# Kernel optimization log

Measured on AMD Instinct MI355X. Metric: run time of the kernel, lower is better.

## Reference

```python
import jax, jax.numpy as jnp
import numpy as np

N_NODES = 50000
N_EDGES = 800000
IN_CH, HID_CH, OUT_CH = 128, 128, 64


def setup_inputs() -> dict:
    key = jax.random.key(0)
    ks = jax.random.split(key, 8)
    x = jax.random.normal(ks[0], (N_NODES, IN_CH), dtype=jnp.float32)
    src = jax.random.randint(ks[1], (N_EDGES,), 0, N_NODES, dtype=jnp.int32)
    dst = jax.random.randint(ks[2], (N_EDGES,), 0, N_NODES, dtype=jnp.int32)
    s1 = 1.0 / np.sqrt(IN_CH)
    s2 = 1.0 / np.sqrt(HID_CH)
    W_self1 = jax.random.normal(ks[3], (IN_CH, HID_CH), dtype=jnp.float32) * s1
    W_neigh1 = jax.random.normal(ks[4], (IN_CH, HID_CH), dtype=jnp.float32) * s1
    b1 = jnp.zeros((HID_CH,), dtype=jnp.float32)
    W_self2 = jax.random.normal(ks[5], (HID_CH, OUT_CH), dtype=jnp.float32) * s2
    W_neigh2 = jax.random.normal(ks[6], (HID_CH, OUT_CH), dtype=jnp.float32) * s2
    b2 = jnp.zeros((OUT_CH,), dtype=jnp.float32)
    return {"x": x, "src": src, "dst": dst,
            "W_self1": W_self1, "W_neigh1": W_neigh1, "b1": b1,
            "W_self2": W_self2, "W_neigh2": W_neigh2, "b2": b2}


def _mean_agg(h, src, dst, inv_deg):
    # gather source features, scatter-sum onto destinations, divide by in-degree
    summed = jax.ops.segment_sum(h[src], dst, num_segments=N_NODES)  # [N, d]
    return summed * inv_deg[:, None]


def _sage_layer(h, src, dst, inv_deg, W_self, W_neigh, b):
    h_neigh = _mean_agg(h, src, dst, inv_deg)
    return h @ W_self + h_neigh @ W_neigh + b


def reference(x, src, dst, W_self1, W_neigh1, b1, W_self2, W_neigh2, b2):
    deg = jax.ops.segment_sum(jnp.ones_like(dst, dtype=x.dtype), dst,
                              num_segments=N_NODES)
    inv_deg = 1.0 / jnp.maximum(deg, 1.0)  # isolated nodes -> 0 neighbor feature
    h = _sage_layer(x, src, dst, inv_deg, W_self1, W_neigh1, b1)
    h = jax.nn.relu(h)
    out = _sage_layer(h, src, dst, inv_deg, W_self2, W_neigh2, b2)
    return out
```

## Files before the change

kernel.cpp:

```cpp
#include <hip/hip_runtime.h>

#define N_CH 128
#define CAP 7680

typedef short bf16x8 __attribute__((ext_vector_type(8)));
typedef float f32x4 __attribute__((ext_vector_type(4)));

__device__ __forceinline__ unsigned short f2bf(float f) {
    unsigned int u = __float_as_uint(f);
    unsigned int r = (u + 0x7fffu + ((u >> 16) & 1u)) >> 16;
    return (unsigned short)r;
}
__device__ __forceinline__ unsigned int pkbf(float a, float b) {
    return (unsigned int)f2bf(a) | ((unsigned int)f2bf(b) << 16);
}
__device__ __forceinline__ float bflo(unsigned int v) { return __uint_as_float(v << 16); }
__device__ __forceinline__ float bfhi(unsigned int v) { return __uint_as_float(v & 0xffff0000u); }

__global__ __launch_bounds__(256) void k_inithist(const float* __restrict__ x,
                                                  const float* __restrict__ Ws1,
                                                  const float* __restrict__ Wn1,
                                                  const float* __restrict__ Ws2,
                                                  const float* __restrict__ Wn2,
                                                  unsigned short* __restrict__ Bt1,
                                                  unsigned short* __restrict__ Bt2,
                                                  uint4* __restrict__ xb4, int nxq, int nxb,
                                                  const int* __restrict__ dst,
                                                  int* __restrict__ H, int e, int nbh,
                                                  int nbkt) {
    __shared__ int hist[256];
    int b = blockIdx.x, t = threadIdx.x;
    if (b < 192) {
        int idx = b * 256 + t;
        if (idx < 128 * 256) {
            int n = idx >> 8, k = idx & 255;
            float v = (k < 128) ? Ws1[k * 128 + n] : Wn1[(k - 128) * 128 + n];
            Bt1[idx] = f2bf(v);
        } else {
            int j = idx - 128 * 256;
            int n = j >> 7, k = j & 127;
            float v = (n < 64) ? Ws2[k * 64 + n] : Wn2[k * 64 + (n - 64)];
            Bt2[j] = f2bf(v);
        }
    } else if (b < 192 + nxb) {
        int q = (b - 192) * 256 + t;
        if (q < nxq) {
            const float4* xf = (const float4*)x;
            float4 f0 = xf[2 * q], f1 = xf[2 * q + 1];
            uint4 o;
            o.x = pkbf(f0.x, f0.y); o.y = pkbf(f0.z, f0.w);
            o.z = pkbf(f1.x, f1.y); o.w = pkbf(f1.z, f1.w);
            xb4[q] = o;
        }
    } else {
        int hb = b - 192 - nxb;
        hist[t] = 0;
        __syncthreads();
        int i = hb * 1024 + t * 4;
        if (i + 3 < e) {
            int4 d4 = *(const int4*)&dst[i];
            atomicAdd(&hist[d4.x >> 8], 1);
            atomicAdd(&hist[d4.y >> 8], 1);
            atomicAdd(&hist[d4.z >> 8], 1);
            atomicAdd(&hist[d4.w >> 8], 1);
        } else {
            for (int j = i; j < e && j < i + 4; ++j) atomicAdd(&hist[dst[j] >> 8], 1);
        }
        __syncthreads();
        if (t < nbkt) H[t * nbh + hb] = hist[t];
    }
}

__global__ __launch_bounds__(256) void k_reduce(const int* __restrict__ H,
                                                int* __restrict__ bsum, int tot) {
    __shared__ int sm[256];
    int i = blockIdx.x * 256 + threadIdx.x;
    sm[threadIdx.x] = (i < tot) ? H[i] : 0;
    __syncthreads();
    for (int s = 128; s > 0; s >>= 1) {
        if (threadIdx.x < s) sm[threadIdx.x] += sm[threadIdx.x + s];
        __syncthreads();
    }
    if (threadIdx.x == 0) bsum[blockIdx.x] = sm[0];
}

__global__ __launch_bounds__(256) void k_scan(const int* __restrict__ H,
                                              const int* __restrict__ bsum,
                                              int* __restrict__ Hs, int tot) {
    __shared__ int sm[256];
    __shared__ int sbase;
    int t = threadIdx.x, b = blockIdx.x;
    int acc = 0;
    for (int j = t; j < b; j += 256) acc += bsum[j];
    sm[t] = acc;
    __syncthreads();
    for (int s = 128; s > 0; s >>= 1) {
        if (t < s) sm[t] += sm[t + s];
        __syncthreads();
    }
    if (t == 0) sbase = sm[0];
    __syncthreads();
    int base = sbase;
    __syncthreads();
    int i = b * 256 + t;
    int v = (i < tot) ? H[i] : 0;
    sm[t] = v;
    __syncthreads();
    for (int off = 1; off < 256; off <<= 1) {
        int add = (t >= off) ? sm[t - off] : 0;
        __syncthreads();
        sm[t] += add;
        __syncthreads();
    }
    if (i < tot) Hs[i] = base + sm[t] - v;
}

__global__ __launch_bounds__(256) void k_scatter1(const int* __restrict__ src,
                                                  const int* __restrict__ dst,
                                                  const int* __restrict__ Hs,
                                                  int* __restrict__ buf,
                                                  int e, int nbh, int nbkt) {
    __shared__ int cur[256];
    int t = threadIdx.x, b = blockIdx.x;
    if (t < nbkt) cur[t] = Hs[t * nbh + b];
    __syncthreads();
    int i = b * 1024 + t * 4;
    if (i + 3 < e) {
        int4 d4 = *(const int4*)&dst[i];
        int4 s4 = *(const int4*)&src[i];
        int r0 = atomicAdd(&cur[d4.x >> 8], 1);
        buf[r0] = ((d4.x & 255) << 16) | s4.x;
        int r1 = atomicAdd(&cur[d4.y >> 8], 1);
        buf[r1] = ((d4.y & 255) << 16) | s4.y;
        int r2 = atomicAdd(&cur[d4.z >> 8], 1);
        buf[r2] = ((d4.z & 255) << 16) | s4.z;
        int r3 = atomicAdd(&cur[d4.w >> 8], 1);
        buf[r3] = ((d4.w & 255) << 16) | s4.w;
    } else {
        for (int j = i; j < e && j < i + 4; ++j) {
            int d = dst[j];
            int r = atomicAdd(&cur[d >> 8], 1);
            buf[r] = ((d & 255) << 16) | src[j];
        }
    }
}

__global__ __launch_bounds__(256) void k_bucket(const int* __restrict__ buf,
                                                const int* __restrict__ Hs,
                                                int* __restrict__ csr_src,
                                                int* __restrict__ deg,
                                                int* __restrict__ row_start,
                                                int e, int nbh, int nbkt, int n) {
    __shared__ int hist[256];
    __shared__ int excl[256];
    __shared__ int cur[256];
    __shared__ int cache[CAP];
    int t = threadIdx.x, b = blockIdx.x;
    int base = Hs[b * nbh];
    int end = (b == nbkt - 1) ? e : Hs[(b + 1) * nbh];
    int cnt = end - base;
    hist[t] = 0;
    __syncthreads();
    for (int i = t; i < cnt; i += 256) {
        int v = buf[base + i];
        if (i < CAP) cache[i] = v;
        atomicAdd(&hist[(v >> 16) & 255], 1);
    }
    __syncthreads();
    int v = hist[t];
    excl[t] = v;
    __syncthreads();
    for (int off = 1; off < 256; off <<= 1) {
        int add = (t >= off) ? excl[t - off] : 0;
        __syncthreads();
        excl[t] += add;
        __syncthreads();
    }
    int ex = excl[t] - v;
    cur[t] = ex;
    int node = b * 256 + t;
    if (node < n) {
        deg[node] = v;
        row_start[node] = base + ex;
    }
    __syncthreads();
    for (int i = t; i < cnt; i += 256) {
        int ed = (i < CAP) ? cache[i] : buf[base + i];
        int r = atomicAdd(&cur[(ed >> 16) & 255], 1);
        csr_src[base + r] = ed & 0xFFFF;
    }
}

__global__ __launch_bounds__(256) void k_aggx(const uint4* __restrict__ xb4,
                                              uint4* __restrict__ xagg4,
                                              const int* __restrict__ row_start,
                                              const int* __restrict__ deg,
                                              const int* __restrict__ csr, int n) {
    int gw = (blockIdx.x * 256 + threadIdx.x) >> 6;
    int lane = threadIdx.x & 63;
    if (gw >= n) return;
    int start = row_start[gw];
    int cnt = deg[gw];
    const int q = lane >> 4;
    const int cl = lane & 15;
    float a0 = 0.f, a1 = 0.f, a2 = 0.f, a3 = 0.f, a4 = 0.f, a5 = 0.f, a6 = 0.f, a7 = 0.f;
    int i = 0;
    for (; i + 16 <= cnt; i += 16) {
        int e0 = csr[start + i + q];
        int e1 = csr[start + i + 4 + q];
        int e2 = csr[start + i + 8 + q];
        int e3 = csr[start + i + 12 + q];
        uint4 v0 = xb4[e0 * 16 + cl];
        uint4 v1 = xb4[e1 * 16 + cl];
        uint4 v2 = xb4[e2 * 16 + cl];
        uint4 v3 = xb4[e3 * 16 + cl];
        a0 += bflo(v0.x) + bflo(v1.x) + bflo(v2.x) + bflo(v3.x);
        a1 += bfhi(v0.x) + bfhi(v1.x) + bfhi(v2.x) + bfhi(v3.x);
        a2 += bflo(v0.y) + bflo(v1.y) + bflo(v2.y) + bflo(v3.y);
        a3 += bfhi(v0.y) + bfhi(v1.y) + bfhi(v2.y) + bfhi(v3.y);
        a4 += bflo(v0.z) + bflo(v1.z) + bflo(v2.z) + bflo(v3.z);
        a5 += bfhi(v0.z) + bfhi(v1.z) + bfhi(v2.z) + bfhi(v3.z);
        a6 += bflo(v0.w) + bflo(v1.w) + bflo(v2.w) + bflo(v3.w);
        a7 += bfhi(v0.w) + bfhi(v1.w) + bfhi(v2.w) + bfhi(v3.w);
    }
    if (i + 8 <= cnt) {
        int e0 = csr[start + i + q];
        int e1 = csr[start + i + 4 + q];
        uint4 v0 = xb4[e0 * 16 + cl];
        uint4 v1 = xb4[e1 * 16 + cl];
        a0 += bflo(v0.x) + bflo(v1.x); a1 += bfhi(v0.x) + bfhi(v1.x);
        a2 += bflo(v0.y) + bflo(v1.y); a3 += bfhi(v0.y) + bfhi(v1.y);
        a4 += bflo(v0.z) + bflo(v1.z); a5 += bfhi(v0.z) + bfhi(v1.z);
        a6 += bflo(v0.w) + bflo(v1.w); a7 += bfhi(v0.w) + bfhi(v1.w);
        i += 8;
    }
    for (; i < cnt; i += 4) {
        int nbi = i + q;
        if (nbi < cnt) {
            uint4 va = xb4[csr[start + nbi] * 16 + cl];
            a0 += bflo(va.x); a1 += bfhi(va.x);
            a2 += bflo(va.y); a3 += bfhi(va.y);
            a4 += bflo(va.z); a5 += bfhi(va.z);
            a6 += bflo(va.w); a7 += bfhi(va.w);
        }
    }
    a0 += __shfl_xor(a0, 16); a0 += __shfl_xor(a0, 32);
    a1 += __shfl_xor(a1, 16); a1 += __shfl_xor(a1, 32);
    a2 += __shfl_xor(a2, 16); a2 += __shfl_xor(a2, 32);
    a3 += __shfl_xor(a3, 16); a3 += __shfl_xor(a3, 32);
    a4 += __shfl_xor(a4, 16); a4 += __shfl_xor(a4, 32);
    a5 += __shfl_xor(a5, 16); a5 += __shfl_xor(a5, 32);
    a6 += __shfl_xor(a6, 16); a6 += __shfl_xor(a6, 32);
    a7 += __shfl_xor(a7, 16); a7 += __shfl_xor(a7, 32);

    float inv = 1.0f / fmaxf((float)cnt, 1.0f);
    if (q == 0) {
        uint4 o;
        o.x = pkbf(inv * a0, inv * a1);
        o.y = pkbf(inv * a2, inv * a3);
        o.z = pkbf(inv * a4, inv * a5);
        o.w = pkbf(inv * a6, inv * a7);
        xagg4[gw * 16 + cl] = o;
    }
}

__global__ __launch_bounds__(256) void k_gemm12(const uint4* __restrict__ xb4,
                                                const uint4* __restrict__ xagg4,
                                                const unsigned short* __restrict__ Bt1,
                                                const float* __restrict__ b1,
                                                const unsigned short* __restrict__ Bt2,
                                                const float* __restrict__ b2,
                                                float* __restrict__ out,
                                                unsigned short* __restrict__ p2, int M) {
    __shared__ unsigned short As[64][256];
    unsigned short* lds = &As[0][0];
    const int m0 = blockIdx.x * 64;
    const int tid = threadIdx.x;
    const int w = tid >> 6;
    const int l = tid & 63;
    const int fr = l & 15;
    const int kq = l >> 4;

    for (int p = tid; p < 2048; p += 256) {
        int row = p >> 5, c = p & 31;
        int gr = m0 + row;
        uint4 v = make_uint4(0, 0, 0, 0);
        if (gr < M) v = (c < 16) ? xb4[gr * 16 + c] : xagg4[gr * 16 + (c - 16)];
        *(uint4*)&As[row][(c ^ (row & 7)) * 8] = v;
    }
    __syncthreads();

    f32x4 acc[2][4] = {};
#pragma unroll
    for (int kt = 0; kt < 8; ++kt) {
        bf16x8 bfr[2];
#pragma unroll
        for (int ct = 0; ct < 2; ++ct) {
            int nn = w * 32 + ct * 16 + fr;
            bfr[ct] = *(const bf16x8*)&Bt1[nn * 256 + kt * 32 + kq * 8];
        }
        bf16x8 af[4];
#pragma unroll
        for (int rt = 0; rt < 4; ++rt) {
            int row = rt * 16 + fr;
            int c = (kt * 4 + kq) ^ (row & 7);
            af[rt] = *(bf16x8*)&As[row][c * 8];
        }
#pragma unroll
        for (int ct = 0; ct < 2; ++ct)
#pragma unroll
            for (int rt = 0; rt < 4; ++rt)
                acc[ct][rt] = __builtin_amdgcn_mfma_f32_16x16x32_bf16(af[rt], bfr[ct],
                                                                      acc[ct][rt], 0, 0, 0);
    }
    __syncthreads();

#pragma unroll
    for (int ct = 0; ct < 2; ++ct) {
        int col = w * 32 + ct * 16 + fr;
        float bv = b1[col];
        int c8 = col >> 3, c7 = col & 7;
#pragma unroll
        for (int rt = 0; rt < 4; ++rt) {
#pragma unroll
            for (int j = 0; j < 4; ++j) {
                int row = rt * 16 + (l >> 4) * 4 + j;
                unsigned short hv = f2bf(fmaxf(acc[ct][rt][j] + bv, 0.f));
                lds[row * 128 + (c8 ^ (row & 7)) * 8 + c7] = hv;
            }
        }
    }
    __syncthreads();

    f32x4 acc2[2][4] = {};
#pragma unroll
    for (int kt = 0; kt < 4; ++kt) {
        bf16x8 bfr[2];
#pragma unroll
        for (int ct = 0; ct < 2; ++ct) {
            int nn = w * 32 + ct * 16 + fr;
            bfr[ct] = *(const bf16x8*)&Bt2[nn * 128 + kt * 32 + kq * 8];
        }
        bf16x8 af[4];
#pragma unroll
        for (int rt = 0; rt < 4; ++rt) {
            int row = rt * 16 + fr;
            int c = (kt * 4 + kq) ^ (row & 7);
            af[rt] = *(bf16x8*)&lds[row * 128 + c * 8];
        }
#pragma unroll
        for (int ct = 0; ct < 2; ++ct)
#pragma unroll
            for (int rt = 0; rt < 4; ++rt)
                acc2[ct][rt] = __builtin_amdgcn_mfma_f32_16x16x32_bf16(af[rt], bfr[ct],
                                                                       acc2[ct][rt], 0, 0, 0);
    }

#pragma unroll
    for (int ct = 0; ct < 2; ++ct) {
        int col = w * 32 + ct * 16 + fr;
        bool isS = col < 64;
        float bv = isS ? b2[col] : 0.f;
#pragma unroll
        for (int rt = 0; rt < 4; ++rt) {
#pragma unroll
            for (int j = 0; j < 4; ++j) {
                int row = m0 + rt * 16 + (l >> 4) * 4 + j;
                if (row < M) {
                    float v = acc2[ct][rt][j];
                    if (isS) out[row * 64 + col] = v + bv;
                    else p2[row * 64 + (col - 64)] = f2bf(v);
                }
            }
        }
    }
}

__global__ __launch_bounds__(256) void k_agg2_add(const unsigned int* __restrict__ p,
                                                  float* __restrict__ out,
                                                  const int* __restrict__ row_start,
                                                  const int* __restrict__ deg,
                                                  const int* __restrict__ csr, int n) {
    int gw = (blockIdx.x * 256 + threadIdx.x) >> 6;
    int lane = threadIdx.x & 63;
    if (gw >= n) return;
    int start = row_start[gw];
    int cnt = deg[gw];
    const int g = lane >> 3;
    const int cl = lane & 7;
    float a0 = 0.f, a1 = 0.f, a2 = 0.f, a3 = 0.f, a4 = 0.f, a5 = 0.f, a6 = 0.f, a7 = 0.f;
    int i = 0;
    for (; i + 16 <= cnt; i += 16) {
        int e0 = csr[start + i + g];
        int e1 = csr[start + i + 8 + g];
        uint4 v0 = *(const uint4*)&p[e0 * 32 + cl * 4];
        uint4 v1 = *(const uint4*)&p[e1 * 32 + cl * 4];
        a0 += bflo(v0.x) + bflo(v1.x); a1 += bfhi(v0.x) + bfhi(v1.x);
        a2 += bflo(v0.y) + bflo(v1.y); a3 += bfhi(v0.y) + bfhi(v1.y);
        a4 += bflo(v0.z) + bflo(v1.z); a5 += bfhi(v0.z) + bfhi(v1.z);
        a6 += bflo(v0.w) + bflo(v1.w); a7 += bfhi(v0.w) + bfhi(v1.w);
    }
    for (; i < cnt; i += 8) {
        int nbi = i + g;
        if (nbi < cnt) {
            int ia = csr[start + nbi];
            uint4 va = *(const uint4*)&p[ia * 32 + cl * 4];
            a0 += bflo(va.x); a1 += bfhi(va.x);
            a2 += bflo(va.y); a3 += bfhi(va.y);
            a4 += bflo(va.z); a5 += bfhi(va.z);
            a6 += bflo(va.w); a7 += bfhi(va.w);
        }
    }
    a0 += __shfl_xor(a0, 8); a0 += __shfl_xor(a0, 16); a0 += __shfl_xor(a0, 32);
    a1 += __shfl_xor(a1, 8); a1 += __shfl_xor(a1, 16); a1 += __shfl_xor(a1, 32);
    a2 += __shfl_xor(a2, 8); a2 += __shfl_xor(a2, 16); a2 += __shfl_xor(a2, 32);
    a3 += __shfl_xor(a3, 8); a3 += __shfl_xor(a3, 16); a3 += __shfl_xor(a3, 32);
    a4 += __shfl_xor(a4, 8); a4 += __shfl_xor(a4, 16); a4 += __shfl_xor(a4, 32);
    a5 += __shfl_xor(a5, 8); a5 += __shfl_xor(a5, 16); a5 += __shfl_xor(a5, 32);
    a6 += __shfl_xor(a6, 8); a6 += __shfl_xor(a6, 16); a6 += __shfl_xor(a6, 32);
    a7 += __shfl_xor(a7, 8); a7 += __shfl_xor(a7, 16); a7 += __shfl_xor(a7, 32);
    float inv = 1.0f / fmaxf((float)cnt, 1.0f);
    if (g == 0) {
        float4 oa = *(const float4*)&out[gw * 64 + cl * 8];
        float4 ob = *(const float4*)&out[gw * 64 + cl * 8 + 4];
        oa.x += inv * a0; oa.y += inv * a1; oa.z += inv * a2; oa.w += inv * a3;
        ob.x += inv * a4; ob.y += inv * a5; ob.z += inv * a6; ob.w += inv * a7;
        *(float4*)&out[gw * 64 + cl * 8] = oa;
        *(float4*)&out[gw * 64 + cl * 8 + 4] = ob;
    }
}

extern "C" void kernel_launch(void* const* d_in, const int* in_sizes, int n_in,
                              void* d_out, int out_size, void* d_ws, size_t ws_size,
                              hipStream_t stream) {
    const float* x   = (const float*)d_in[0];
    const int*   src = (const int*)d_in[1];
    const int*   dst = (const int*)d_in[2];
    const float* Ws1 = (const float*)d_in[3];
    const float* Wn1 = (const float*)d_in[4];
    const float* b1  = (const float*)d_in[5];
    const float* Ws2 = (const float*)d_in[6];
    const float* Wn2 = (const float*)d_in[7];
    const float* b2  = (const float*)d_in[8];
    float* out = (float*)d_out;
    const int N = in_sizes[0] / N_CH;
    const int E = in_sizes[1];

    const int nbh  = (E + 1023) / 1024;
    const int nbkt = (N + 255) / 256;
    const int htot = nbkt * nbh;
    const int nb2  = (htot + 255) / 256;
    const int nxq  = N * 16;
    const int nxb  = (nxq + 255) / 256;

    char* ws = (char*)d_ws;
    int* deg       = (int*)(ws + 0);
    int* row_start = (int*)(ws + 200704);
    int* bsum2     = (int*)(ws + 401408);
    int* csr_src   = (int*)(ws + 403968);
    int* H         = (int*)(ws + 3603968);
    int* Hs        = (int*)(ws + 4217344);
    int* buf       = (int*)(ws + 4830720);
    unsigned short* xb   = (unsigned short*)(ws + 8030720);
    unsigned short* xagg = (unsigned short*)(ws + 20830720);
    unsigned short* p2   = (unsigned short*)(ws + 33630720);
    unsigned short* Bt1  = (unsigned short*)(ws + 40030720);
    unsigned short* Bt2  = (unsigned short*)(ws + 40096256);

    k_inithist<<<192 + nxb + nbh, 256, 0, stream>>>(x, Ws1, Wn1, Ws2, Wn2, Bt1, Bt2,
                                                    (uint4*)xb, nxq, nxb, dst, H, E, nbh, nbkt);
    k_reduce<<<nb2, 256, 0, stream>>>(H, bsum2, htot);
    k_scan<<<nb2, 256, 0, stream>>>(H, bsum2, Hs, htot);
    k_scatter1<<<nbh, 256, 0, stream>>>(src, dst, Hs, buf, E, nbh, nbkt);
    k_bucket<<<nbkt, 256, 0, stream>>>(buf, Hs, csr_src, deg, row_start, E, nbh, nbkt, N);

    k_aggx<<<(N + 3) / 4, 256, 0, stream>>>((const uint4*)xb, (uint4*)xagg, row_start, deg,
                                            csr_src, N);

    const int gb = (N + 63) / 64;
    k_gemm12<<<gb, 256, 0, stream>>>((const uint4*)xb, (const uint4*)xagg, Bt1, b1, Bt2, b2,
                                     out, p2, N);
    k_agg2_add<<<(N + 3) / 4, 256, 0, stream>>>((const unsigned int*)p2, out, row_start, deg,
                                                csr_src, N);
}
```

Measured before the change: 111.9 us.

## Move x bf16 cast into scatter kernel and store CSR sources as 16-bit

The x-to-bf16 conversion blocks move out of the histogram kernel and into the scatter kernel, which becomes a combined launch. This shortens the critical early histogram/scan chain and overlaps the cast with the scatter work. CSR source indices are now stored as unsigned short instead of int, halving index traffic in both aggregation kernels. The 16-bit indices only hold while node ids stay below 65536, which is true for the fixed 50000-node graph but not in general.

```diff
diff --git a/kernel.cpp b/kernel.cpp
--- a/kernel.cpp
+++ b/kernel.cpp
@@ -17,14 +17,12 @@
 __device__ __forceinline__ float bflo(unsigned int v) { return __uint_as_float(v << 16); }
 __device__ __forceinline__ float bfhi(unsigned int v) { return __uint_as_float(v & 0xffff0000u); }
 
-__global__ __launch_bounds__(256) void k_inithist(const float* __restrict__ x,
-                                                  const float* __restrict__ Ws1,
+__global__ __launch_bounds__(256) void k_inithist(const float* __restrict__ Ws1,
                                                   const float* __restrict__ Wn1,
                                                   const float* __restrict__ Ws2,
                                                   const float* __restrict__ Wn2,
                                                   unsigned short* __restrict__ Bt1,
                                                   unsigned short* __restrict__ Bt2,
-                                                  uint4* __restrict__ xb4, int nxq, int nxb,
                                                   const int* __restrict__ dst,
                                                   int* __restrict__ H, int e, int nbh,
                                                   int nbkt) {
@@ -42,18 +40,8 @@
             float v = (n < 64) ? Ws2[k * 64 + n] : Wn2[k * 64 + (n - 64)];
             Bt2[j] = f2bf(v);
         }
-    } else if (b < 192 + nxb) {
-        int q = (b - 192) * 256 + t;
-        if (q < nxq) {
-            const float4* xf = (const float4*)x;
-            float4 f0 = xf[2 * q], f1 = xf[2 * q + 1];
-            uint4 o;
-            o.x = pkbf(f0.x, f0.y); o.y = pkbf(f0.z, f0.w);
-            o.z = pkbf(f1.x, f1.y); o.w = pkbf(f1.z, f1.w);
-            xb4[q] = o;
-        }
     } else {
-        int hb = b - 192 - nxb;
+        int hb = b - 192;
         hist[t] = 0;
         __syncthreads();
         int i = hb * 1024 + t * 4;
@@ -115,39 +103,53 @@
     if (i < tot) Hs[i] = base + sm[t] - v;
 }
 
-__global__ __launch_bounds__(256) void k_scatter1(const int* __restrict__ src,
+__global__ __launch_bounds__(256) void k_scatcast(const int* __restrict__ src,
                                                   const int* __restrict__ dst,
                                                   const int* __restrict__ Hs,
                                                   int* __restrict__ buf,
-                                                  int e, int nbh, int nbkt) {
+                                                  int e, int nbh, int nbkt,
+                                                  const float* __restrict__ x,
+                                                  uint4* __restrict__ xb4, int nxq) {
     __shared__ int cur[256];
     int t = threadIdx.x, b = blockIdx.x;
-    if (t < nbkt) cur[t] = Hs[t * nbh + b];
-    __syncthreads();
-    int i = b * 1024 + t * 4;
-    if (i + 3 < e) {
-        int4 d4 = *(const int4*)&dst[i];
-        int4 s4 = *(const int4*)&src[i];
-        int r0 = atomicAdd(&cur[d4.x >> 8], 1);
-        buf[r0] = ((d4.x & 255) << 16) | s4.x;
-        int r1 = atomicAdd(&cur[d4.y >> 8], 1);
-        buf[r1] = ((d4.y & 255) << 16) | s4.y;
-        int r2 = atomicAdd(&cur[d4.z >> 8], 1);
-        buf[r2] = ((d4.z & 255) << 16) | s4.z;
-        int r3 = atomicAdd(&cur[d4.w >> 8], 1);
-        buf[r3] = ((d4.w & 255) << 16) | s4.w;
+    if (b < nbh) {
+        if (t < nbkt) cur[t] = Hs[t * nbh + b];
+        __syncthreads();
+        int i = b * 1024 + t * 4;
+        if (i + 3 < e) {
+            int4 d4 = *(const int4*)&dst[i];
+            int4 s4 = *(const int4*)&src[i];
+            int r0 = atomicAdd(&cur[d4.x >> 8], 1);
+            buf[r0] = ((d4.x & 255) << 16) | s4.x;
+            int r1 = atomicAdd(&cur[d4.y >> 8], 1);
+            buf[r1] = ((d4.y & 255) << 16) | s4.y;
+            int r2 = atomicAdd(&cur[d4.z >> 8], 1);
+            buf[r2] = ((d4.z & 255) << 16) | s4.z;
+            int r3 = atomicAdd(&cur[d4.w >> 8], 1);
+            buf[r3] = ((d4.w & 255) << 16) | s4.w;
+        } else {
+            for (int j = i; j < e && j < i + 4; ++j) {
+                int d = dst[j];
+                int r = atomicAdd(&cur[d >> 8], 1);
+                buf[r] = ((d & 255) << 16) | src[j];
+            }
+        }
     } else {
-        for (int j = i; j < e && j < i + 4; ++j) {
-            int d = dst[j];
-            int r = atomicAdd(&cur[d >> 8], 1);
-            buf[r] = ((d & 255) << 16) | src[j];
+        int q = (b - nbh) * 256 + t;
+        if (q < nxq) {
+            const float4* xf = (const float4*)x;
+            float4 f0 = xf[2 * q], f1 = xf[2 * q + 1];
+            uint4 o;
+            o.x = pkbf(f0.x, f0.y); o.y = pkbf(f0.z, f0.w);
+            o.z = pkbf(f1.x, f1.y); o.w = pkbf(f1.z, f1.w);
+            xb4[q] = o;
         }
     }
 }
 
 __global__ __launch_bounds__(256) void k_bucket(const int* __restrict__ buf,
                                                 const int* __restrict__ Hs,
-                                                int* __restrict__ csr_src,
+                                                unsigned short* __restrict__ csr_src,
                                                 int* __restrict__ deg,
                                                 int* __restrict__ row_start,
                                                 int e, int nbh, int nbkt, int n) {
@@ -187,7 +189,7 @@
     for (int i = t; i < cnt; i += 256) {
         int ed = (i < CAP) ? cache[i] : buf[base + i];
         int r = atomicAdd(&cur[(ed >> 16) & 255], 1);
-        csr_src[base + r] = ed & 0xFFFF;
+        csr_src[base + r] = (unsigned short)(ed & 0xFFFF);
     }
 }
 
@@ -195,7 +197,7 @@
                                               uint4* __restrict__ xagg4,
                                               const int* __restrict__ row_start,
                                               const int* __restrict__ deg,
-                                              const int* __restrict__ csr, int n) {
+                                              const unsigned short* __restrict__ csr, int n) {
     int gw = (blockIdx.x * 256 + threadIdx.x) >> 6;
     int lane = threadIdx.x & 63;
     if (gw >= n) return;
@@ -380,7 +382,8 @@
                                                   float* __restrict__ out,
                                                   const int* __restrict__ row_start,
                                                   const int* __restrict__ deg,
-                                                  const int* __restrict__ csr, int n) {
+                                                  const unsigned short* __restrict__ csr,
+                                                  int n) {
     int gw = (blockIdx.x * 256 + threadIdx.x) >> 6;
     int lane = threadIdx.x & 63;
     if (gw >= n) return;
@@ -457,21 +460,22 @@
     int* deg       = (int*)(ws + 0);
     int* row_start = (int*)(ws + 200704);
     int* bsum2     = (int*)(ws + 401408);
-    int* csr_src   = (int*)(ws + 403968);
-    int* H         = (int*)(ws + 3603968);
-    int* Hs        = (int*)(ws + 4217344);
-    int* buf       = (int*)(ws + 4830720);
-    unsigned short* xb   = (unsigned short*)(ws + 8030720);
-    unsigned short* xagg = (unsigned short*)(ws + 20830720);
-    unsigned short* p2   = (unsigned short*)(ws + 33630720);
-    unsigned short* Bt1  = (unsigned short*)(ws + 40030720);
-    unsigned short* Bt2  = (unsigned short*)(ws + 40096256);
-
-    k_inithist<<<192 + nxb + nbh, 256, 0, stream>>>(x, Ws1, Wn1, Ws2, Wn2, Bt1, Bt2,
-                                                    (uint4*)xb, nxq, nxb, dst, H, E, nbh, nbkt);
+    unsigned short* csr_src = (unsigned short*)(ws + 403968);
+    int* H         = (int*)(ws + 2003968);
+    int* Hs        = (int*)(ws + 2617344);
+    int* buf       = (int*)(ws + 3230720);
+    unsigned short* xb   = (unsigned short*)(ws + 6430720);
+    unsigned short* xagg = (unsigned short*)(ws + 19230720);
+    unsigned short* p2   = (unsigned short*)(ws + 32030720);
+    unsigned short* Bt1  = (unsigned short*)(ws + 38430720);
+    unsigned short* Bt2  = (unsigned short*)(ws + 38496256);
+
+    k_inithist<<<192 + nbh, 256, 0, stream>>>(Ws1, Wn1, Ws2, Wn2, Bt1, Bt2, dst, H, E, nbh,
+                                              nbkt);
     k_reduce<<<nb2, 256, 0, stream>>>(H, bsum2, htot);
     k_scan<<<nb2, 256, 0, stream>>>(H, bsum2, Hs, htot);
-    k_scatter1<<<nbh, 256, 0, stream>>>(src, dst, Hs, buf, E, nbh, nbkt);
+    k_scatcast<<<nbh + nxb, 256, 0, stream>>>(src, dst, Hs, buf, E, nbh, nbkt, x, (uint4*)xb,
+                                              nxq);
     k_bucket<<<nbkt, 256, 0, stream>>>(buf, Hs, csr_src, deg, row_start, E, nbh, nbkt, N);
 
     k_aggx<<<(N + 3) / 4, 256, 0, stream>>>((const uint4*)xb, (uint4*)xagg, row_start, deg,
```

New measurement: 112.4 us. Within noise of the previous version (+0.5%).
